# Optimization experiments

Measured on AMD Instinct MI355X. Metric: run time of the kernel, lower is better.

The kernel has to match this reference:

```python
import jax, jax.numpy as jnp
import numpy as np
from jax import lax

PH = PW = 7  # patch size


def _unfold2d(x, ph, pw):
    # x: [B, C, H, W] -> patches [B*Ho*Wo, C*ph*pw], channel-major like F.unfold
    B, C, H, W = x.shape
    patches = lax.conv_general_dilated_patches(
        x, filter_shape=(ph, pw), window_strides=(1, 1), padding='VALID')
    # patches: [B, C*ph*pw, Ho, Wo] with feature order (c, i, j) matching F.unfold
    Ho, Wo = H - ph + 1, W - pw + 1
    D = C * ph * pw
    q2d = patches.reshape(B, D, Ho * Wo).transpose(0, 2, 1).reshape(B * Ho * Wo, D)
    return q2d, (B, C, H, W, Ho, Wo, D)


def _fold2d_mean(res, shape_info):
    # res: [B*Ho*Wo, D] patch values -> overlap-add mean image [B, C, H, W]
    B, C, H, W, Ho, Wo, D = shape_info
    res = res.reshape(B, Ho, Wo, C, PH, PW)
    out = jnp.zeros((B, C, H, W), dtype=res.dtype)
    cnt = jnp.zeros((H, W), dtype=res.dtype)
    for di in range(PH):          # small fixed 7x7 loop over patch offsets
        for dj in range(PW):
            out = out.at[:, :, di:di + Ho, dj:dj + Wo].add(
                res[:, :, :, :, di, dj].transpose(0, 3, 1, 2))
            cnt = cnt.at[di:di + Ho, dj:dj + Wo].add(1.0)
    return out / cnt  # reduce='mean'


def setup_inputs() -> dict:
    key = jax.random.key(0)
    k1, k2, k3 = jax.random.split(key, 3)
    query = jax.random.normal(k1, (1, 3, 96, 96), dtype=jnp.float32)
    kmat = jax.random.normal(k2, (8100, 147), dtype=jnp.float32)
    vmat = jax.random.normal(k3, (8100, 147), dtype=jnp.float32)
    return {"query": query, "key": kmat, "value": vmat}


def reference(query, key, value):
    # 1) unfold query image into patch rows [Nq, D]
    q2d, shape_info = _unfold2d(query, PH, PW)
    # 2) nearest-neighbor lookup: squared-euclidean argmin over key rows
    qn = jnp.sum(q2d * q2d, axis=1, keepdims=True)        # [Nq, 1]
    kn = jnp.sum(key * key, axis=1)                       # [Nk]
    dist = qn + kn[None, :] - 2.0 * (q2d @ key.T)         # [Nq, Nk]
    idx = jnp.argmin(dist, axis=1)                        # [Nq]
    # 3) gather matched value patches and fold back (overlap-add mean)
    res = value[idx]                                      # [Nq, D]
    return _fold2d_mean(res, shape_info)
```

## Files before the change

### kernel.cpp

```cpp
#include <hip/hip_runtime.h>


#define NQ 8100
#define NK 8100
#define DD 147
#define HO 90
#define IMG 96
#define NCH 5
#define CST 262144
#define ARRN (NCH * CST)

typedef _Float16 half8 __attribute__((ext_vector_type(8)));
typedef float f32x4 __attribute__((ext_vector_type(4)));

__device__ __forceinline__ void gld16(const _Float16* g, _Float16* l) {
    __builtin_amdgcn_global_load_lds(
        (const __attribute__((address_space(1))) unsigned int*)g,
        (__attribute__((address_space(3))) unsigned int*)l, 16, 0, 0);
}

__global__ void k_prep(const float* __restrict__ query, const float* __restrict__ key,
                       _Float16* __restrict__ Qh, _Float16* __restrict__ Ql,
                       _Float16* __restrict__ Kh, _Float16* __restrict__ Kl,
                       float* __restrict__ kn, unsigned long long* __restrict__ fidx64) {
    const int bx = blockIdx.x;
    const bool isK = (blockIdx.y != 0);

    if (bx >= 640) {
        if (!isK) return;
        int wave = threadIdx.x >> 6, lane = threadIdx.x & 63;
        int kb = ((bx - 640) * 4 + wave) * 16;
        for (int r = 0; r < 16; ++r) {
            int k = kb + r;
            float s = 0.f;
            if (k < NK)
                for (int d = lane; d < DD; d += 64) {
                    float v = key[k * DD + d];
                    s += v * v;
                }
#pragma unroll
            for (int off = 32; off; off >>= 1) s += __shfl_down(s, off, 64);
            if (lane == 0) {
                kn[k] = (k < NK) ? s : 1e30f;
                fidx64[k] = 0xFFFFFFFFFFFFFFFFull;
            }
        }
        return;
    }

    int t = bx * 256 + threadIdx.x;
    int c = t >> 15;
    int rem = t & 32767;
    int col = ((rem >> 6) << 4) + (rem & 15);
    int quad = (rem >> 4) & 3;
    int kbase = c * 32 + quad * 8;

    float v[8];
#pragma unroll
    for (int j = 0; j < 8; ++j) {
        int k = kbase + j;
        float x = 0.f;
        if (k < DD && col < NQ) {
            if (isK) {
                x = key[col * DD + k];
            } else {
                int c3 = k / 49, r2 = k - 49 * c3;
                int rr = r2 / 7, ss = r2 - 7 * rr;
                int y = col / HO, xx = col - HO * y;
                x = query[(c3 * IMG + y + rr) * IMG + xx + ss];
            }
        }
        v[j] = x;
    }
    half8 h8, l8;
#pragma unroll
    for (int j = 0; j < 8; ++j) {
        _Float16 h = (_Float16)v[j];
        h8[j] = h;
        l8[j] = (_Float16)((v[j] - (float)h) * 2048.0f);
    }
    if (isK) {
        *(half8*)(Kh + t * 8) = h8;
        *(half8*)(Kl + t * 8) = l8;
    } else {
        *(half8*)(Qh + t * 8) = h8;
        *(half8*)(Ql + t * 8) = l8;
    }
}

__launch_bounds__(256, 2)
__global__ void k_nn(const _Float16* __restrict__ Qh, const _Float16* __restrict__ Ql,
                     const _Float16* __restrict__ Kh, const _Float16* __restrict__ Kl,
                     const float* __restrict__ kn, unsigned long long* __restrict__ out) {
    __shared__ __align__(16) char smem[65536];
    _Float16* sbase = (_Float16*)smem;

    const int tid = (int)threadIdx.x;
    const int wave = tid >> 6, lane = tid & 63;
    const int l15 = lane & 15, quad = lane >> 4;

    const int b = (int)blockIdx.x;
    const int xcd = b & 7;
    const int i = b >> 3;
    const int qt = (xcd >> 1) * 16 + (i & 15);
    const int kt = (xcd & 1) * 32 + (i >> 4);

    const int mbase = (wave >> 1) * 64;
    const int nbase = (wave & 1) * 64;
    const int q0 = qt * 128, n0 = kt * 128;

    const _Float16* gsrc = (wave == 0) ? Qh : (wave == 1) ? Ql : (wave == 2) ? Kh : Kl;
    const int gbase = ((wave < 2) ? qt : kt) * 8;
    const _Float16* gp0 = gsrc + gbase * 512 + lane * 8;
    _Float16* ldst0 = sbase + wave * 4096 + lane * 8;

    f32x4 acc0[4][4], acc1[4][4];
#pragma unroll
    for (int ii = 0; ii < 4; ++ii)
#pragma unroll
        for (int j = 0; j < 4; ++j) {
            acc0[ii][j] = (f32x4)0.f;
            acc1[ii][j] = (f32x4)0.f;
        }

    const int agrp = (mbase >> 4);
    const int bgrp = (nbase >> 4);

#pragma unroll
    for (int grp = 0; grp < 8; ++grp)
        gld16(gp0 + grp * 512, ldst0 + grp * 512);

#pragma unroll
    for (int c = 0; c < NCH; ++c) {
        __syncthreads();
        if (c + 1 < NCH) {
            const _Float16* gp = gp0 + (c + 1) * CST;
            _Float16* ld = ldst0 + ((c + 1) & 1) * 16384;
#pragma unroll
            for (int grp = 0; grp < 8; ++grp)
                gld16(gp + grp * 512, ld + grp * 512);
        }

        const _Float16* sQh = sbase + (c & 1) * 16384;
        const _Float16* sQl = sQh + 4096;
        const _Float16* sKh = sQh + 8192;
        const _Float16* sKl = sQh + 12288;

        __builtin_amdgcn_s_setprio(1);
        half8 ah[4], al[4];
#pragma unroll
        for (int mt = 0; mt < 4; ++mt) {
            int aoff = (agrp + mt) * 512 + lane * 8;
            ah[mt] = *(const half8*)(sQh + aoff);
            al[mt] = *(const half8*)(sQl + aoff);
        }
#pragma unroll
        for (int nt = 0; nt < 4; ++nt) {
            int boff = (bgrp + nt) * 512 + lane * 8;
            half8 bh = *(const half8*)(sKh + boff);
            half8 bl = *(const half8*)(sKl + boff);
#pragma unroll
            for (int mt = 0; mt < 4; ++mt) {
                acc0[mt][nt] = __builtin_amdgcn_mfma_f32_16x16x32_f16(ah[mt], bh, acc0[mt][nt], 0, 0, 0);
                acc1[mt][nt] = __builtin_amdgcn_mfma_f32_16x16x32_f16(ah[mt], bl, acc1[mt][nt], 0, 0, 0);
                acc1[mt][nt] = __builtin_amdgcn_mfma_f32_16x16x32_f16(al[mt], bh, acc1[mt][nt], 0, 0, 0);
            }
        }
        __builtin_amdgcn_s_setprio(0);
    }

    float knv[4];
    int nglob[4];
#pragma unroll
    for (int nt = 0; nt < 4; ++nt) {
        nglob[nt] = n0 + nbase + nt * 16 + l15;
        knv[nt] = kn[nglob[nt]];
    }
    __syncthreads();
    unsigned long long* redu = (unsigned long long*)smem;

#pragma unroll
    for (int mt = 0; mt < 4; ++mt)
#pragma unroll
        for (int r = 0; r < 4; ++r) {
            float bv = 1e38f;
            int bn = 0x7fffffff;
#pragma unroll
            for (int nt = 0; nt < 4; ++nt) {
                float d = knv[nt] - 2.0f * (acc0[mt][nt][r] + acc1[mt][nt][r] * (1.0f / 2048.0f));
                if (d < bv) { bv = d; bn = nglob[nt]; }
            }
            int m = mbase + mt * 16 + quad * 4 + r;
            int cidx = (nbase >> 2) + l15;
            unsigned u = __float_as_uint(bv);
            u = (u & 0x80000000u) ? ~u : (u | 0x80000000u);
            redu[m * 33 + cidx] = ((unsigned long long)u << 32) | (unsigned)bn;
        }
    __syncthreads();

    {
        int row = tid >> 1;
        int base = (tid & 1) * 16;
        unsigned long long best = 0xFFFFFFFFFFFFFFFFull;
        const unsigned long long* rp = redu + row * 33 + base;
#pragma unroll
        for (int t2 = 0; t2 < 16; ++t2) {
            unsigned long long v = rp[t2];
            best = (v < best) ? v : best;
        }
        unsigned long long other = __shfl_xor(best, 1, 64);
        best = (other < best) ? other : best;
        if (!(tid & 1)) atomicMin(&out[q0 + row], best);
    }
}

__global__ void k_fold(const float* __restrict__ value,
                       const unsigned long long* __restrict__ fidx64,
                       float* __restrict__ out) {
    int t = blockIdx.x * 256 + threadIdx.x;
    int pix = t >> 3, s = t & 7;
    if (pix >= 3 * IMG * IMG) return;
    int c = pix / (IMG * IMG);
    int rem = pix % (IMG * IMG);
    int Y = rem / IMG, X = rem % IMG;

    float partial = 0.f;
    int yy = Y - s;
    if (s < 7 && (unsigned)yy < (unsigned)HO) {
        const unsigned* fidx32 = (const unsigned*)fidx64;
        const float* vbase = value + c * 49 + s * 7;
        int rows[7];
        bool oks[7];
#pragma unroll
        for (int j = 0; j < 7; ++j) {
            int xx = X - j;
            bool ok = (unsigned)xx < (unsigned)HO;
            int p = ok ? (yy * HO + xx) : 0;
            rows[j] = (int)fidx32[2 * p];
            oks[j] = ok;
        }
#pragma unroll
        for (int j = 0; j < 7; ++j) {
            float v = vbase[rows[j] * DD + j];
            if (oks[j]) partial += v;
        }
    }
    partial += __shfl_down(partial, 4, 8);
    partial += __shfl_down(partial, 2, 8);
    partial += __shfl_down(partial, 1, 8);
    if (s == 0) {
        int i0 = max(0, Y - (HO - 1)), i1 = min(6, Y);
        int j0 = max(0, X - (HO - 1)), j1 = min(6, X);
        float cnt = (float)((i1 - i0 + 1) * (j1 - j0 + 1));
        out[pix] = partial / cnt;
    }
}

extern "C" void kernel_launch(void* const* d_in, const int* in_sizes, int n_in,
                              void* d_out, int out_size, void* d_ws, size_t ws_size,
                              hipStream_t stream) {
    const float* query = (const float*)d_in[0];
    const float* key   = (const float*)d_in[1];
    const float* value = (const float*)d_in[2];
    float* out = (float*)d_out;

    _Float16* Qh = (_Float16*)d_ws;
    _Float16* Ql = Qh + ARRN;
    _Float16* Kh = Ql + ARRN;
    _Float16* Kl = Kh + ARRN;
    float* kn = (float*)(Kl + ARRN);
    unsigned long long* fidx64 = (unsigned long long*)(kn + 8192);

    dim3 gp(768, 2);
    k_prep<<<gp, 256, 0, stream>>>(query, key, Qh, Ql, Kh, Kl, kn, fidx64);
    k_nn<<<4096, 256, 0, stream>>>(Qh, Ql, Kh, Kl, kn, fidx64);
    k_fold<<<864, 256, 0, stream>>>(value, fidx64, out);
}
```

Measured before the change: 146.4 us.

## Load MFMA operand fragments directly from global memory, dropping LDS staging

Removes the double-buffered global-to-LDS async staging and its per-chunk barriers. Each wave now loads its A and B half8 fragments straight from global memory into registers, and shared memory shrinks to the size the reduction needs. The intent is to cut barrier and LDS round-trip overhead and to allow more blocks per CU. The cost is that each fragment is read from global/L2 twice, once by each wave sharing it, and load latency is no longer overlapped by explicit prefetch. Removing the __syncthreads before redu is safe only because redu no longer aliases the staging buffers.

```diff
diff --git a/kernel.cpp b/kernel.cpp
--- a/kernel.cpp
+++ b/kernel.cpp
@@ -12,12 +12,6 @@
 
 typedef _Float16 half8 __attribute__((ext_vector_type(8)));
 typedef float f32x4 __attribute__((ext_vector_type(4)));
-
-__device__ __forceinline__ void gld16(const _Float16* g, _Float16* l) {
-    __builtin_amdgcn_global_load_lds(
-        (const __attribute__((address_space(1))) unsigned int*)g,
-        (__attribute__((address_space(3))) unsigned int*)l, 16, 0, 0);
-}
 
 __global__ void k_prep(const float* __restrict__ query, const float* __restrict__ key,
                        _Float16* __restrict__ Qh, _Float16* __restrict__ Ql,
@@ -92,8 +86,7 @@
 __global__ void k_nn(const _Float16* __restrict__ Qh, const _Float16* __restrict__ Ql,
                      const _Float16* __restrict__ Kh, const _Float16* __restrict__ Kl,
                      const float* __restrict__ kn, unsigned long long* __restrict__ out) {
-    __shared__ __align__(16) char smem[65536];
-    _Float16* sbase = (_Float16*)smem;
+    __shared__ __align__(16) char smem[33792];
 
     const int tid = (int)threadIdx.x;
     const int wave = tid >> 6, lane = tid & 63;
@@ -109,10 +102,12 @@
     const int nbase = (wave & 1) * 64;
     const int q0 = qt * 128, n0 = kt * 128;
 
-    const _Float16* gsrc = (wave == 0) ? Qh : (wave == 1) ? Ql : (wave == 2) ? Kh : Kl;
-    const int gbase = ((wave < 2) ? qt : kt) * 8;
-    const _Float16* gp0 = gsrc + gbase * 512 + lane * 8;
-    _Float16* ldst0 = sbase + wave * 4096 + lane * 8;
+    const int agrp = (mbase >> 4);
+    const int bgrp = (nbase >> 4);
+    const _Float16* gQh = Qh + (qt * 8 + agrp) * 512 + lane * 8;
+    const _Float16* gQl = Ql + (qt * 8 + agrp) * 512 + lane * 8;
+    const _Float16* gKh = Kh + (kt * 8 + bgrp) * 512 + lane * 8;
+    const _Float16* gKl = Kl + (kt * 8 + bgrp) * 512 + lane * 8;
 
     f32x4 acc0[4][4], acc1[4][4];
 #pragma unroll
@@ -123,47 +118,28 @@
             acc1[ii][j] = (f32x4)0.f;
         }
 
-    const int agrp = (mbase >> 4);
-    const int bgrp = (nbase >> 4);
-
-#pragma unroll
-    for (int grp = 0; grp < 8; ++grp)
-        gld16(gp0 + grp * 512, ldst0 + grp * 512);
-
 #pragma unroll
     for (int c = 0; c < NCH; ++c) {
-        __syncthreads();
-        if (c + 1 < NCH) {
-            const _Float16* gp = gp0 + (c + 1) * CST;
-            _Float16* ld = ldst0 + ((c + 1) & 1) * 16384;
-#pragma unroll
-            for (int grp = 0; grp < 8; ++grp)
-                gld16(gp + grp * 512, ld + grp * 512);
-        }
-
-        const _Float16* sQh = sbase + (c & 1) * 16384;
-        const _Float16* sQl = sQh + 4096;
-        const _Float16* sKh = sQh + 8192;
-        const _Float16* sKl = sQh + 12288;
+        half8 ah[4], al[4], bh[4], bl[4];
+#pragma unroll
+        for (int mt = 0; mt < 4; ++mt) {
+            ah[mt] = *(const half8*)(gQh + c * CST + mt * 512);
+            al[mt] = *(const half8*)(gQl + c * CST + mt * 512);
+        }
+#pragma unroll
+        for (int nt = 0; nt < 4; ++nt) {
+            bh[nt] = *(const half8*)(gKh + c * CST + nt * 512);
+            bl[nt] = *(const half8*)(gKl + c * CST + nt * 512);
+        }
 
         __builtin_amdgcn_s_setprio(1);
-        half8 ah[4], al[4];
-#pragma unroll
-        for (int mt = 0; mt < 4; ++mt) {
-            int aoff = (agrp + mt) * 512 + lane * 8;
-            ah[mt] = *(const half8*)(sQh + aoff);
-            al[mt] = *(const half8*)(sQl + aoff);
-        }
 #pragma unroll
         for (int nt = 0; nt < 4; ++nt) {
-            int boff = (bgrp + nt) * 512 + lane * 8;
-            half8 bh = *(const half8*)(sKh + boff);
-            half8 bl = *(const half8*)(sKl + boff);
 #pragma unroll
             for (int mt = 0; mt < 4; ++mt) {
-                acc0[mt][nt] = __builtin_amdgcn_mfma_f32_16x16x32_f16(ah[mt], bh, acc0[mt][nt], 0, 0, 0);
-                acc1[mt][nt] = __builtin_amdgcn_mfma_f32_16x16x32_f16(ah[mt], bl, acc1[mt][nt], 0, 0, 0);
-                acc1[mt][nt] = __builtin_amdgcn_mfma_f32_16x16x32_f16(al[mt], bh, acc1[mt][nt], 0, 0, 0);
+                acc0[mt][nt] = __builtin_amdgcn_mfma_f32_16x16x32_f16(ah[mt], bh[nt], acc0[mt][nt], 0, 0, 0);
+                acc1[mt][nt] = __builtin_amdgcn_mfma_f32_16x16x32_f16(ah[mt], bl[nt], acc1[mt][nt], 0, 0, 0);
+                acc1[mt][nt] = __builtin_amdgcn_mfma_f32_16x16x32_f16(al[mt], bh[nt], acc1[mt][nt], 0, 0, 0);
             }
         }
         __builtin_amdgcn_s_setprio(0);
@@ -176,7 +152,6 @@
         nglob[nt] = n0 + nbase + nt * 16 + l15;
         knv[nt] = kn[nglob[nt]];
     }
-    __syncthreads();
     unsigned long long* redu = (unsigned long long*)smem;
 
 #pragma unroll
```

Result: no change. 144.2 us (-1.5%).
